# Kernel tuning notes

Hardware: AMD Instinct MI355X
Metric: run time of the kernel (lower is better)

Reference implementation:

```python
import jax, jax.numpy as jnp
import numpy as np
from functools import partial

B, DIN, H, D, HW = 4096, 2048, 1024, 256, 256
MAX_STEPS = 15
STEP = 1.0 / MAX_STEPS
WEIGHT = 1.0


def safe_norm(x):
    # per-sample L2 norm, keepdims, nan-safe at 0
    return jnp.sqrt(jnp.sum(x * x, axis=-1, keepdims=True) + 1e-24)


def setup_inputs() -> dict:
    key = jax.random.key(0)
    ks = jax.random.split(key, 16)
    s = lambda fan: 1.0 / np.sqrt(fan)
    inp = {
        'x_start': jax.random.normal(ks[0], (B, DIN), jnp.float32),
        'x_end': jax.random.normal(ks[1], (B, DIN), jnp.float32),
        'noise_raw': jax.random.normal(ks[2], (B, D), jnp.float32),
        # encoder params
        'W1': jax.random.normal(ks[3], (DIN, H), jnp.float32) * s(DIN),
        'b1': jnp.zeros((H,), jnp.float32),
        'W2': jax.random.normal(ks[4], (H, D), jnp.float32) * s(H),
        'b2': jnp.zeros((D,), jnp.float32),
        # Zermelo wind field params
        'Ww1': jax.random.normal(ks[5], (D, HW), jnp.float32) * s(D),
        'bw1': jnp.zeros((HW,), jnp.float32),
        'Ww2': jax.random.normal(ks[6], (HW, D), jnp.float32) * s(HW),
        'bw2': jnp.zeros((D,), jnp.float32),
        # conformal potential phi params (metric g = exp(phi) I)
        'Wp1': jax.random.normal(ks[7], (D, HW), jnp.float32) * s(D),
        'bp1': jnp.zeros((HW,), jnp.float32),
        'wp2': jax.random.normal(ks[8], (HW,), jnp.float32) * s(HW),
    }
    return inp


def _encode(x, W1, b1, W2, b2):
    return jnp.tanh(x @ W1 + b1) @ W2 + b2  # [B, D]


def _wind(z, Ww1, bw1, Ww2, bw2):
    return jnp.tanh(z @ Ww1 + bw1) @ Ww2 + bw2  # [B, D]


def _grad_phi(x, Wp1, bp1, wp2):
    # phi(x) = wp2 . tanh(x @ Wp1 + bp1); analytic gradient, fully vectorized
    h = jnp.tanh(x @ Wp1 + bp1)          # [B, HW]
    return ((1.0 - h * h) * wp2) @ Wp1.T  # [B, D]


def _accel(x, v, Wp1, bp1, wp2):
    # geodesic spray of conformal metric e^{phi} I:
    # a = -(grad_phi . v) v + 0.5 |v|^2 grad_phi
    g = _grad_phi(x, Wp1, bp1, wp2)
    gv = jnp.sum(g * v, axis=-1, keepdims=True)
    vv = jnp.sum(v * v, axis=-1, keepdims=True)
    return -gv * v + 0.5 * vv * g


def _trace(z0, v0, Wp1, bp1, wp2):
    h = STEP
    acc = partial(_accel, Wp1=Wp1, bp1=bp1, wp2=wp2)

    def step(carry, _):
        x, v = carry
        k1x, k1v = v, acc(x, v)
        k2x, k2v = v + 0.5 * h * k1v, acc(x + 0.5 * h * k1x, v + 0.5 * h * k1v)
        k3x, k3v = v + 0.5 * h * k2v, acc(x + 0.5 * h * k2x, v + 0.5 * h * k2v)
        k4x, k4v = v + h * k3v, acc(x + h * k3x, v + h * k3v)
        xn = x + (h / 6.0) * (k1x + 2 * k2x + 2 * k3x + k4x)
        vn = v + (h / 6.0) * (k1v + 2 * k2v + 2 * k3v + k4v)
        return (xn, vn), xn

    (_, _), xs = jax.lax.scan(step, (z0, v0), None, length=MAX_STEPS)
    return xs  # [MAX_STEPS, B, D] == xs[1:] of the original trace


def reference(x_start, x_end, noise_raw, W1, b1, W2, b2,
              Ww1, bw1, Ww2, bw2, Wp1, bp1, wp2):
    z_s = _encode(x_start, W1, b1, W2, b2)
    z_e = _encode(x_end, W1, b1, W2, b2)
    W_start = _wind(z_s, Ww1, bw1, Ww2, bw2)
    # degenerate-wind fallback: tiny tangent noise (Euclidean manifold -> identity projection)
    noise = noise_raw / (safe_norm(noise_raw) + 1e-12) * 1e-4
    w_norm = safe_norm(W_start)  # [B, 1]
    W_start = jnp.where(w_norm < 1e-5, W_start + noise, W_start)
    xs = _trace(z_s, W_start, Wp1, bp1, wp2)          # [S, B, D]
    dists_sq = jnp.sum((xs - z_e) ** 2, axis=-1)      # [S, B]
    min_dist_sq = jnp.min(dists_sq, axis=0)           # closest approach per sample
    return jnp.mean(min_dist_sq) * WEIGHT
```

## Files before the change

kernel.cpp:

```cpp
#include <hip/hip_runtime.h>
#include <math.h>

typedef short bf8 __attribute__((ext_vector_type(8)));
typedef short s4v __attribute__((ext_vector_type(4)));
typedef float f32x4 __attribute__((ext_vector_type(4)));

namespace {

constexpr float H_STEP = 1.0f / 15.0f;

__device__ inline short f2bf(float f) {
  unsigned u = __float_as_uint(f);
  u += 0x7fffu + ((u >> 16) & 1u);
  return (short)(u >> 16);
}

__device__ inline float fast_tanh(float x) {
  const float ax = fabsf(x);
  const float e = __expf(-2.0f * ax);
  const float t = (1.0f - e) * __builtin_amdgcn_rcpf(1.0f + e);
  return copysignf(t, x);
}

__device__ inline float sech2(float x) {
  const float e = __expf(-2.0f * fabsf(x));
  const float r = __builtin_amdgcn_rcpf(1.0f + e);
  return 4.0f * e * r * r;
}

template <int CTRL>
__device__ inline float dppadd(float v) {
  return v + __int_as_float(__builtin_amdgcn_update_dpp(
                 0, __float_as_int(v), CTRL, 0xF, 0xF, true));
}
__device__ inline float red16(float v) {
  v = dppadd<0x121>(v);
  v = dppadd<0x122>(v);
  v = dppadd<0x124>(v);
  v = dppadd<0x128>(v);
  return v;
}

__device__ inline void async16(const void* g, void* l) {
  __builtin_amdgcn_global_load_lds((__attribute__((address_space(1))) void*)g,
                                   (__attribute__((address_space(3))) void*)l,
                                   16, 0, 0);
}

__device__ inline void stpk4(short* base, int byteoff, float a, float b,
                             float c, float d) {
  unsigned lo, hi;
  asm("v_cvt_pk_bf16_f32 %0, %1, %2" : "=v"(lo) : "v"(a), "v"(b));
  asm("v_cvt_pk_bf16_f32 %0, %1, %2" : "=v"(hi) : "v"(c), "v"(d));
  uint2 u;
  u.x = lo;
  u.y = hi;
  *(uint2*)((char*)base + byteoff) = u;
}

__global__ __launch_bounds__(256) void prep_all(
    const float* __restrict__ xs, const float* __restrict__ xe,
    const float* __restrict__ W1, const float* __restrict__ W2,
    const float* __restrict__ Ww1, const float* __restrict__ Ww2,
    const float* __restrict__ Wp1, const float* __restrict__ wp2,
    short* __restrict__ XSb, short* __restrict__ W1T, short* __restrict__ W2T,
    short* __restrict__ Ww1T, short* __restrict__ Ww2T,
    short* __restrict__ WpT, short* __restrict__ Wp1s,
    float* __restrict__ outz) {
  __shared__ float tile[32][33];
  const int id = blockIdx.x;
  if (id < 2048) {
    if (id == 0 && threadIdx.x == 0) *outz = 0.0f;
    const long n = (long)8192 * 2048, half = n >> 1;
    long i = ((long)id * 256 + threadIdx.x) * 4;
    const long stride = (long)2048 * 1024;
    for (; i < n; i += stride) {
      const float* s = (i < half) ? (xs + i) : (xe + (i - half));
      const float4 f = *(const float4*)s;
      ushort4 o;
      o.x = (unsigned short)f2bf(f.x);
      o.y = (unsigned short)f2bf(f.y);
      o.z = (unsigned short)f2bf(f.z);
      o.w = (unsigned short)f2bf(f.w);
      *(ushort4*)(XSb + i) = o;
    }
    return;
  }
  const int tr = threadIdx.x >> 5, tc = threadIdx.x & 31;
  const float* src;
  short* dst;
  int K, N, kt, nt;
  if (id < 4096) {
    src = W1; dst = W1T; K = 2048; N = 1024; kt = (id - 2048) >> 5; nt = (id - 2048) & 31;
  } else if (id < 4352) {
    src = W2; dst = W2T; K = 1024; N = 256; kt = (id - 4096) >> 3; nt = (id - 4096) & 7;
  } else if (id < 4416) {
    src = Ww1; dst = Ww1T; K = 256; N = 256; kt = (id - 4352) >> 3; nt = (id - 4352) & 7;
  } else if (id < 4480) {
    src = Ww2; dst = Ww2T; K = 256; N = 256; kt = (id - 4416) >> 3; nt = (id - 4416) & 7;
  } else if (id < 4544) {
    src = Wp1; dst = WpT; K = 256; N = 256; kt = (id - 4480) >> 3; nt = (id - 4480) & 7;
  } else {
    const int lid = id - 4544;
    const int k0 = (lid >> 3) * 32, n0 = (lid & 7) * 32;
#pragma unroll
    for (int i = 0; i < 32; i += 8) {
      const size_t o = (size_t)(k0 + tr + i) * 256 + n0 + tc;
      Wp1s[o] = f2bf(Wp1[o] * wp2[n0 + tc]);
    }
    return;
  }
  const int k0 = kt * 32, n0 = nt * 32;
#pragma unroll
  for (int i = 0; i < 32; i += 8)
    tile[tr + i][tc] = src[(size_t)(k0 + tr + i) * N + n0 + tc];
  __syncthreads();
#pragma unroll
  for (int i = 0; i < 32; i += 8)
    dst[(size_t)(n0 + tr + i) * K + k0 + tc] = f2bf(tile[tc][tr + i]);
}


__global__ __launch_bounds__(256) void gemm128_tanh(
    const short* __restrict__ A, const short* __restrict__ Bt,
    const float* __restrict__ bias, short* __restrict__ Cb, int M, int N,
    int K) {
  __shared__ __align__(16) short As[2 * 128 * 32];
  __shared__ __align__(16) short Bs[2 * 128 * 32];
  const int tid = threadIdx.x;
  const int w = tid >> 6, lane = tid & 63, q = lane >> 4, l15 = lane & 15;
  const int wm = (w >> 1) * 64, wn = (w & 1) * 64;
  const int m0 = blockIdx.y * 128, n0 = blockIdx.x * 128;
  const f32x4 fzero = {0.0f, 0.0f, 0.0f, 0.0f};
  f32x4 acc[4][4];
#pragma unroll
  for (int mt = 0; mt < 4; ++mt)
#pragma unroll
    for (int nt = 0; nt < 4; ++nt) acc[mt][nt] = fzero;

  for (int k0 = 0; k0 < K; k0 += 64) {
#pragma unroll
    for (int kcb = 0; kcb < 2; ++kcb)
#pragma unroll
      for (int j = 0; j < 2; ++j) {
        const int c = w * 128 + j * 64 + lane;
        async16(A + (size_t)(m0 + (c >> 2)) * K + k0 + kcb * 32 + (c & 3) * 8,
                &As[kcb * 4096 + (w * 128 + j * 64) * 8]);
        async16(Bt + (size_t)(n0 + (c >> 2)) * K + k0 + kcb * 32 + (c & 3) * 8,
                &Bs[kcb * 4096 + (w * 128 + j * 64) * 8]);
      }
    __syncthreads();
#pragma unroll
    for (int kcb = 0; kcb < 2; ++kcb) {
      bf8 af[4], bfr[4];
#pragma unroll
      for (int mt = 0; mt < 4; ++mt)
        af[mt] =
            *(const bf8*)&As[kcb * 4096 + (wm + mt * 16 + l15) * 32 + q * 8];
#pragma unroll
      for (int nt = 0; nt < 4; ++nt)
        bfr[nt] =
            *(const bf8*)&Bs[kcb * 4096 + (wn + nt * 16 + l15) * 32 + q * 8];
#pragma unroll
      for (int mt = 0; mt < 4; ++mt)
#pragma unroll
        for (int nt = 0; nt < 4; ++nt)
          acc[mt][nt] = __builtin_amdgcn_mfma_f32_16x16x32_bf16(
              af[mt], bfr[nt], acc[mt][nt], 0, 0, 0);
    }
    __syncthreads();
  }
#pragma unroll
  for (int mt = 0; mt < 4; ++mt)
#pragma unroll
    for (int nt = 0; nt < 4; ++nt) {
      const int col = n0 + wn + nt * 16 + l15;
      const float bcol = bias[col];
#pragma unroll
      for (int rg = 0; rg < 4; ++rg) {
        const int row = m0 + wm + mt * 16 + q * 4 + rg;
        Cb[(size_t)row * N + col] = f2bf(fast_tanh(acc[mt][nt][rg] + bcol));
      }
    }
}

__global__ __launch_bounds__(256) void gemm64_enc2(
    const short* __restrict__ A, const short* __restrict__ Bt,
    const float* __restrict__ bias, float* __restrict__ Zs,
    float* __restrict__ Ze, int M, int N, int K) {
  __shared__ __align__(16) short As[2 * 64 * 32];
  __shared__ __align__(16) short Bs[2 * 64 * 32];
  const int tid = threadIdx.x;
  const int w = tid >> 6, lane = tid & 63, q = lane >> 4, l15 = lane & 15;
  const int wm = (w >> 1) * 32, wn = (w & 1) * 32;
  const int m0 = blockIdx.y * 64, n0 = blockIdx.x * 64;
  const f32x4 fzero = {0.0f, 0.0f, 0.0f, 0.0f};
  f32x4 acc[2][2];
#pragma unroll
  for (int mt = 0; mt < 2; ++mt)
#pragma unroll
    for (int nt = 0; nt < 2; ++nt) acc[mt][nt] = fzero;

  for (int k0 = 0; k0 < K; k0 += 64) {
    const int c = w * 64 + lane;
#pragma unroll
    for (int kcb = 0; kcb < 2; ++kcb) {
      async16(A + (size_t)(m0 + (c >> 2)) * K + k0 + kcb * 32 + (c & 3) * 8,
              &As[kcb * 2048 + (w * 64) * 8]);
      async16(Bt + (size_t)(n0 + (c >> 2)) * K + k0 + kcb * 32 + (c & 3) * 8,
              &Bs[kcb * 2048 + (w * 64) * 8]);
    }
    __syncthreads();
#pragma unroll
    for (int kcb = 0; kcb < 2; ++kcb) {
      bf8 af[2], bfr[2];
#pragma unroll
      for (int mt = 0; mt < 2; ++mt)
        af[mt] =
            *(const bf8*)&As[kcb * 2048 + (wm + mt * 16 + l15) * 32 + q * 8];
#pragma unroll
      for (int nt = 0; nt < 2; ++nt)
        bfr[nt] =
            *(const bf8*)&Bs[kcb * 2048 + (wn + nt * 16 + l15) * 32 + q * 8];
#pragma unroll
      for (int mt = 0; mt < 2; ++mt)
#pragma unroll
        for (int nt = 0; nt < 2; ++nt)
          acc[mt][nt] = __builtin_amdgcn_mfma_f32_16x16x32_bf16(
              af[mt], bfr[nt], acc[mt][nt], 0, 0, 0);
    }
    __syncthreads();
  }
#pragma unroll
  for (int mt = 0; mt < 2; ++mt)
#pragma unroll
    for (int nt = 0; nt < 2; ++nt) {
      const int col = n0 + wn + nt * 16 + l15;
      const float bcol = bias[col];
#pragma unroll
      for (int rg = 0; rg < 4; ++rg) {
        const int row = m0 + wm + mt * 16 + q * 4 + rg;
        const float val = acc[mt][nt][rg] + bcol;
        if (row < 4096)
          Zs[(size_t)row * N + col] = val;
        else
          Ze[(size_t)(row - 4096) * N + col] = val;
      }
    }
}


__global__ __launch_bounds__(512, 2) void trace_fused(
    const float* __restrict__ Xg, const float* __restrict__ ZEg,
    const float* __restrict__ NZg, const short* __restrict__ WT,
    const short* __restrict__ Wp1s, const short* __restrict__ Ww1T,
    const short* __restrict__ Ww2T, const float* __restrict__ bw1,
    const float* __restrict__ bw2, const float* __restrict__ bp1,
    float* __restrict__ out) {
  constexpr float hs = H_STEP;
  __shared__ __align__(16) short XsL[4096];
  __shared__ __align__(16) short UL[4096];
  __shared__ __align__(16) float gvv[2][16][2];
  __shared__ __align__(16) float db[2][16];
  const int tid = threadIdx.x;
  const int w = tid >> 6, lane = tid & 63, q = lane >> 4, l15 = lane & 15;
  const int r0 = blockIdx.x * 16;
  const int col0 = w * 32 + q * 4;
  const int wrow = w * 32 + l15;

  if (tid < 16) {
    *(float2*)gvv[0][tid] = make_float2(0.f, 0.f);
    *(float2*)gvv[1][tid] = make_float2(0.f, 0.f);
    db[0][tid] = 0.f;
    db[1][tid] = 0.f;
  }

  const int smask = ((l15 >> 1) & 7) ^ ((l15 & 1) << 2);
  int wadrT[2], radrT[8];
#pragma unroll
  for (int t = 0; t < 2; ++t) {
    const int slot = w * 4 + t * 2 + (q >> 1);
    wadrT[t] = (l15 * 32 + (slot ^ smask)) * 16 + (q & 1) * 8;
  }
#pragma unroll
  for (int ks = 0; ks < 8; ++ks)
    radrT[ks] = (l15 * 32 + ((ks * 4 + q) ^ smask)) * 16;

  float x[2][4], ze[2][4], nz[2][4];
#pragma unroll
  for (int t = 0; t < 2; ++t) {
    const size_t off = (size_t)(r0 + l15) * 256 + col0 + t * 16;
    const float4 xa = *(const float4*)(Xg + off);
    const float4 za = *(const float4*)(ZEg + off);
    const float4 na = *(const float4*)(NZg + off);
    x[t][0] = xa.x; x[t][1] = xa.y; x[t][2] = xa.z; x[t][3] = xa.w;
    ze[t][0] = za.x; ze[t][1] = za.y; ze[t][2] = za.z; ze[t][3] = za.w;
    nz[t][0] = na.x; nz[t][1] = na.y; nz[t][2] = na.z; nz[t][3] = na.w;
  }
  float bp1c[2][4];
#pragma unroll
  for (int t = 0; t < 2; ++t) {
    const float4 pa = *(const float4*)(bp1 + col0 + t * 16);
    bp1c[t][0] = pa.x; bp1c[t][1] = pa.y; bp1c[t][2] = pa.z; bp1c[t][3] = pa.w;
  }
  const f32x4 fzero = {0.0f, 0.0f, 0.0f, 0.0f};

  float v[2][4];
  {
    bf8 Wf1[2][8], Wf2[2][8];
#pragma unroll
    for (int t = 0; t < 2; ++t)
#pragma unroll
      for (int ks = 0; ks < 8; ++ks) {
        Wf1[t][ks] =
            *(const bf8*)(Ww1T + (size_t)(wrow + t * 16) * 256 + ks * 32 + q * 8);
        Wf2[t][ks] =
            *(const bf8*)(Ww2T + (size_t)(wrow + t * 16) * 256 + ks * 32 + q * 8);
      }
    float bw1c[2][4], bw2c[2][4];
#pragma unroll
    for (int t = 0; t < 2; ++t) {
      const float4 a1 = *(const float4*)(bw1 + col0 + t * 16);
      const float4 a2 = *(const float4*)(bw2 + col0 + t * 16);
      bw1c[t][0] = a1.x; bw1c[t][1] = a1.y; bw1c[t][2] = a1.z; bw1c[t][3] = a1.w;
      bw2c[t][0] = a2.x; bw2c[t][1] = a2.y; bw2c[t][2] = a2.z; bw2c[t][3] = a2.w;
    }
#pragma unroll
    for (int t = 0; t < 2; ++t)
      stpk4(XsL, wadrT[t], x[t][0], x[t][1], x[t][2], x[t][3]);
    __syncthreads();
    bf8 af[8];
#pragma unroll
    for (int ks = 0; ks < 8; ++ks)
      af[ks] = *(const bf8*)((const char*)XsL + radrT[ks]);
    f32x4 acc[2];
#pragma unroll
    for (int t = 0; t < 2; ++t) {
      f32x4 a0 = fzero, a1 = fzero;
#pragma unroll
      for (int ks = 0; ks < 8; ks += 2) {
        a0 = __builtin_amdgcn_mfma_f32_16x16x32_bf16(Wf1[t][ks], af[ks], a0, 0,
                                                     0, 0);
        a1 = __builtin_amdgcn_mfma_f32_16x16x32_bf16(Wf1[t][ks + 1],
                                                     af[ks + 1], a1, 0, 0, 0);
      }
      acc[t] = a0 + a1;
    }
#pragma unroll
    for (int t = 0; t < 2; ++t)
      stpk4(UL, wadrT[t], fast_tanh(acc[t][0] + bw1c[t][0]),
            fast_tanh(acc[t][1] + bw1c[t][1]),
            fast_tanh(acc[t][2] + bw1c[t][2]),
            fast_tanh(acc[t][3] + bw1c[t][3]));
    __syncthreads();
#pragma unroll
    for (int ks = 0; ks < 8; ++ks)
      af[ks] = *(const bf8*)((const char*)UL + radrT[ks]);
#pragma unroll
    for (int t = 0; t < 2; ++t) {
      f32x4 a0 = fzero, a1 = fzero;
#pragma unroll
      for (int ks = 0; ks < 8; ks += 2) {
        a0 = __builtin_amdgcn_mfma_f32_16x16x32_bf16(Wf2[t][ks], af[ks], a0, 0,
                                                     0, 0);
        a1 = __builtin_amdgcn_mfma_f32_16x16x32_bf16(Wf2[t][ks + 1],
                                                     af[ks + 1], a1, 0, 0, 0);
      }
      acc[t] = a0 + a1;
#pragma unroll
      for (int rg = 0; rg < 4; ++rg) v[t][rg] = acc[t][rg] + bw2c[t][rg];
    }
    float pn = 0.f, pm = 0.f;
#pragma unroll
    for (int t = 0; t < 2; ++t)
#pragma unroll
      for (int rg = 0; rg < 4; ++rg) {
        pn = fmaf(v[t][rg], v[t][rg], pn);
        pm = fmaf(nz[t][rg], nz[t][rg], pm);
      }
    pn += __shfl_xor(pn, 16);
    pn += __shfl_xor(pn, 32);
    pm += __shfl_xor(pm, 16);
    pm += __shfl_xor(pm, 32);
    if (q == 0) {
      atomicAdd(&gvv[0][l15][0], pn);
      atomicAdd(&gvv[0][l15][1], pm);
    }
    __syncthreads();
    const float wn = sqrtf(gvv[0][l15][0] + 1e-24f);
    const float sc =
        (wn < 1e-5f) ? 1e-4f / (sqrtf(gvv[0][l15][1] + 1e-24f) + 1e-12f) : 0.0f;
#pragma unroll
    for (int t = 0; t < 2; ++t)
#pragma unroll
      for (int rg = 0; rg < 4; ++rg) v[t][rg] = fmaf(sc, nz[t][rg], v[t][rg]);
    __syncthreads();
    if (tid < 16) *(float2*)gvv[0][tid] = make_float2(0.f, 0.f);
    __syncthreads();
  }

  bf8 B1f[2][8], B2f[2][8];
#pragma unroll
  for (int t = 0; t < 2; ++t)
#pragma unroll
    for (int ks = 0; ks < 8; ++ks) {
      B1f[t][ks] =
          *(const bf8*)(WT + (size_t)(wrow + t * 16) * 256 + ks * 32 + q * 8);
      B2f[t][ks] =
          *(const bf8*)(Wp1s + (size_t)(wrow + t * 16) * 256 + ks * 32 + q * 8);
    }
  float ap[2][4], xacc[2][4], vacc[2][4];
#pragma unroll
  for (int t = 0; t < 2; ++t)
#pragma unroll
    for (int rg = 0; rg < 4; ++rg) ap[t][rg] = 0.0f;
  float md = 3.4e38f;
  const float cxv_t[4] = {0.0f, 0.5f * hs, 0.5f * hs, hs};
  const float cxa_t[4] = {0.0f, 0.0f, 0.25f * hs * hs, 0.5f * hs * hs};
  const float cva_t[4] = {0.0f, 0.5f * hs, 0.5f * hs, hs};

#pragma unroll 1
  for (int step = 0; step < 15; ++step) {
#pragma unroll
    for (int st = 0; st < 4; ++st) {
      const int p = st & 1;
      const float cxv = cxv_t[st], cxa = cxa_t[st], cva = cva_t[st];
      float vs[2][4], pv = 0.f;
#pragma unroll
      for (int t = 0; t < 2; ++t) {
        float sx[4];
#pragma unroll
        for (int rg = 0; rg < 4; ++rg) {
          vs[t][rg] = fmaf(cva, ap[t][rg], v[t][rg]);
          sx[rg] = x[t][rg] + cxv * v[t][rg] + cxa * ap[t][rg];
          pv = fmaf(vs[t][rg], vs[t][rg], pv);
        }
        stpk4(XsL, wadrT[t], sx[0], sx[1], sx[2], sx[3]);
      }
      pv += __shfl_xor(pv, 16);
      pv += __shfl_xor(pv, 32);
      if (q == 0) atomicAdd(&gvv[p][l15][1], pv);
      __syncthreads();
      if (st == 0 && step > 0) md = fminf(md, db[(step - 1) & 1][l15]);
      bf8 af[8];
#pragma unroll
      for (int ks = 0; ks < 8; ++ks)
        af[ks] = *(const bf8*)((const char*)XsL + radrT[ks]);
      f32x4 acc[2];
#pragma unroll
      for (int t = 0; t < 2; ++t) {
        f32x4 a0 = fzero, a1 = fzero;
#pragma unroll
        for (int ks = 0; ks < 8; ks += 2) {
          a0 = __builtin_amdgcn_mfma_f32_16x16x32_bf16(B1f[t][ks], af[ks], a0,
                                                       0, 0, 0);
          a1 = __builtin_amdgcn_mfma_f32_16x16x32_bf16(B1f[t][ks + 1],
                                                       af[ks + 1], a1, 0, 0,
                                                       0);
        }
        acc[t] = a0 + a1;
        stpk4(UL, wadrT[t], sech2(acc[t][0] + bp1c[t][0]),
              sech2(acc[t][1] + bp1c[t][1]), sech2(acc[t][2] + bp1c[t][2]),
              sech2(acc[t][3] + bp1c[t][3]));
      }
      if (tid < 16) *(float2*)gvv[p ^ 1][tid] = make_float2(0.f, 0.f);
      __syncthreads();
      if (st == 0 && step > 0 && tid < 16) db[(step - 1) & 1][tid] = 0.0f;
#pragma unroll
      for (int ks = 0; ks < 8; ++ks)
        af[ks] = *(const bf8*)((const char*)UL + radrT[ks]);
#pragma unroll
      for (int t = 0; t < 2; ++t) {
        f32x4 a0 = fzero, a1 = fzero;
#pragma unroll
        for (int ks = 0; ks < 8; ks += 2) {
          a0 = __builtin_amdgcn_mfma_f32_16x16x32_bf16(B2f[t][ks], af[ks], a0,
                                                       0, 0, 0);
          a1 = __builtin_amdgcn_mfma_f32_16x16x32_bf16(B2f[t][ks + 1],
                                                       af[ks + 1], a1, 0, 0,
                                                       0);
        }
        acc[t] = a0 + a1;
      }
      float pg = 0.f;
#pragma unroll
      for (int t = 0; t < 2; ++t)
#pragma unroll
        for (int rg = 0; rg < 4; ++rg) pg = fmaf(acc[t][rg], vs[t][rg], pg);
      pg += __shfl_xor(pg, 16);
      pg += __shfl_xor(pg, 32);
      if (q == 0) atomicAdd(&gvv[p][l15][0], pg);
      __syncthreads();
      const float2 r2 = *(const float2*)gvv[p][l15];
      const float gv = r2.x, vv = r2.y;
#pragma unroll
      for (int t = 0; t < 2; ++t)
#pragma unroll
        for (int rg = 0; rg < 4; ++rg) {
          const float a = -gv * vs[t][rg] + 0.5f * vv * acc[t][rg];
          ap[t][rg] = a;
          if (st == 0) {
            xacc[t][rg] = a;
            vacc[t][rg] = a;
          } else if (st < 3) {
            xacc[t][rg] += a;
            vacc[t][rg] += 2.0f * a;
          } else {
            vacc[t][rg] += a;
          }
        }
      if (st == 3) {
        const int sp = step & 1;
        float pd = 0.f;
#pragma unroll
        for (int t = 0; t < 2; ++t)
#pragma unroll
          for (int rg = 0; rg < 4; ++rg) {
            const float xn =
                x[t][rg] + hs * v[t][rg] + (hs * hs / 6.0f) * xacc[t][rg];
            const float vn = v[t][rg] + (hs / 6.0f) * vacc[t][rg];
            x[t][rg] = xn;
            v[t][rg] = vn;
            const float dd = xn - ze[t][rg];
            pd = fmaf(dd, dd, pd);
          }
        pd += __shfl_xor(pd, 16);
        pd += __shfl_xor(pd, 32);
        if (q == 0) atomicAdd(&db[sp][l15], pd);
      }
    }
  }
  __syncthreads();
  md = fminf(md, db[14 & 1][l15]);
  if (w == 0) {
    const float s = red16(md);
    if (tid == 0) atomicAdd(out, s * (1.0f / 4096.0f));
  }
}

}

extern "C" void kernel_launch(void* const* d_in, const int* in_sizes, int n_in,
                              void* d_out, int out_size, void* d_ws,
                              size_t ws_size, hipStream_t stream) {
  (void)in_sizes; (void)n_in; (void)out_size; (void)ws_size;
  const float* x_start = (const float*)d_in[0];
  const float* x_end = (const float*)d_in[1];
  const float* noise = (const float*)d_in[2];
  const float* W1 = (const float*)d_in[3];
  const float* b1 = (const float*)d_in[4];
  const float* W2 = (const float*)d_in[5];
  const float* b2 = (const float*)d_in[6];
  const float* Ww1 = (const float*)d_in[7];
  const float* bw1 = (const float*)d_in[8];
  const float* Ww2 = (const float*)d_in[9];
  const float* bw2 = (const float*)d_in[10];
  const float* Wp1 = (const float*)d_in[11];
  const float* bp1 = (const float*)d_in[12];
  const float* wp2 = (const float*)d_in[13];
  float* out = (float*)d_out;

  float* Xf = (float*)d_ws;
  float* ZEf = Xf + (size_t)4096 * 256;
  short* XSb = (short*)(ZEf + (size_t)4096 * 256);
  short* H1b = XSb + (size_t)8192 * 2048;
  short* W1T = H1b + (size_t)8192 * 1024;
  short* W2T = W1T + (size_t)1024 * 2048;
  short* Ww1T = W2T + (size_t)256 * 1024;
  short* Ww2T = Ww1T + 65536;
  short* WpT = Ww2T + 65536;
  short* Wp1s = WpT + 65536;

  const dim3 blk(256);

  prep_all<<<4608, blk, 0, stream>>>(x_start, x_end, W1, W2, Ww1, Ww2, Wp1,
                                     wp2, XSb, W1T, W2T, Ww1T, Ww2T, WpT,
                                     Wp1s, out);
  gemm128_tanh<<<dim3(8, 64), blk, 0, stream>>>(XSb, W1T, b1, H1b, 8192, 1024,
                                                2048);
  gemm64_enc2<<<dim3(4, 128), blk, 0, stream>>>(H1b, W2T, b2, Xf, ZEf, 8192,
                                                256, 1024);
  trace_fused<<<256, dim3(512), 0, stream>>>(Xf, ZEf, noise, WpT, Wp1s, Ww1T,
                                             Ww2T, bw1, bw2, bp1, out);
}
```

Before: 315.7 us.

## Split trace_fused work across 16 waves with one 16-column tile each

Doubles the trace kernel's block size from 512 to 1024 threads, so each wave owns one 16-column output tile instead of two. This halves per-thread register state (weight fragments, x/v accumulators) and doubles the number of waves available to hide MFMA and LDS latency within the sequential RK4 loop. In exchange, every barrier and shared-memory atomic reduction now synchronises 16 waves instead of 8, and launch bounds request 4 waves per SIMD, which limits registers per thread.

New measurement: 349.6 us. +10.7%, slower.

```diff
diff --git a/kernel.cpp b/kernel.cpp
--- a/kernel.cpp
+++ b/kernel.cpp
@@ -2,7 +2,6 @@
 #include <math.h>
 
 typedef short bf8 __attribute__((ext_vector_type(8)));
-typedef short s4v __attribute__((ext_vector_type(4)));
 typedef float f32x4 __attribute__((ext_vector_type(4)));
 
 namespace {
@@ -250,7 +249,7 @@
 }
 
 
-__global__ __launch_bounds__(512, 2) void trace_fused(
+__global__ __launch_bounds__(1024, 4) void trace_fused(
     const float* __restrict__ Xg, const float* __restrict__ ZEg,
     const float* __restrict__ NZg, const short* __restrict__ WT,
     const short* __restrict__ Wp1s, const short* __restrict__ Ww1T,
@@ -265,8 +264,8 @@
   const int tid = threadIdx.x;
   const int w = tid >> 6, lane = tid & 63, q = lane >> 4, l15 = lane & 15;
   const int r0 = blockIdx.x * 16;
-  const int col0 = w * 32 + q * 4;
-  const int wrow = w * 32 + l15;
+  const int col0 = w * 16 + q * 4;
+  const int wrow = w * 16 + l15;
 
   if (tid < 16) {
     *(float2*)gvv[0][tid] = make_float2(0.f, 0.f);
@@ -276,108 +275,88 @@
   }
 
   const int smask = ((l15 >> 1) & 7) ^ ((l15 & 1) << 2);
-  int wadrT[2], radrT[8];
-#pragma unroll
-  for (int t = 0; t < 2; ++t) {
-    const int slot = w * 4 + t * 2 + (q >> 1);
-    wadrT[t] = (l15 * 32 + (slot ^ smask)) * 16 + (q & 1) * 8;
-  }
+  const int wadr =
+      (l15 * 32 + ((w * 2 + (q >> 1)) ^ smask)) * 16 + (q & 1) * 8;
+  int radrT[8];
 #pragma unroll
   for (int ks = 0; ks < 8; ++ks)
     radrT[ks] = (l15 * 32 + ((ks * 4 + q) ^ smask)) * 16;
 
-  float x[2][4], ze[2][4], nz[2][4];
-#pragma unroll
-  for (int t = 0; t < 2; ++t) {
-    const size_t off = (size_t)(r0 + l15) * 256 + col0 + t * 16;
+  float x[4], ze[4], nz[4];
+  {
+    const size_t off = (size_t)(r0 + l15) * 256 + col0;
     const float4 xa = *(const float4*)(Xg + off);
     const float4 za = *(const float4*)(ZEg + off);
     const float4 na = *(const float4*)(NZg + off);
-    x[t][0] = xa.x; x[t][1] = xa.y; x[t][2] = xa.z; x[t][3] = xa.w;
-    ze[t][0] = za.x; ze[t][1] = za.y; ze[t][2] = za.z; ze[t][3] = za.w;
-    nz[t][0] = na.x; nz[t][1] = na.y; nz[t][2] = na.z; nz[t][3] = na.w;
-  }
-  float bp1c[2][4];
-#pragma unroll
-  for (int t = 0; t < 2; ++t) {
-    const float4 pa = *(const float4*)(bp1 + col0 + t * 16);
-    bp1c[t][0] = pa.x; bp1c[t][1] = pa.y; bp1c[t][2] = pa.z; bp1c[t][3] = pa.w;
+    x[0] = xa.x; x[1] = xa.y; x[2] = xa.z; x[3] = xa.w;
+    ze[0] = za.x; ze[1] = za.y; ze[2] = za.z; ze[3] = za.w;
+    nz[0] = na.x; nz[1] = na.y; nz[2] = na.z; nz[3] = na.w;
+  }
+  float bp1c[4];
+  {
+    const float4 pa = *(const float4*)(bp1 + col0);
+    bp1c[0] = pa.x; bp1c[1] = pa.y; bp1c[2] = pa.z; bp1c[3] = pa.w;
   }
   const f32x4 fzero = {0.0f, 0.0f, 0.0f, 0.0f};
 
-  float v[2][4];
+  float v[4];
   {
-    bf8 Wf1[2][8], Wf2[2][8];
-#pragma unroll
-    for (int t = 0; t < 2; ++t)
-#pragma unroll
-      for (int ks = 0; ks < 8; ++ks) {
-        Wf1[t][ks] =
-            *(const bf8*)(Ww1T + (size_t)(wrow + t * 16) * 256 + ks * 32 + q * 8);
-        Wf2[t][ks] =
-            *(const bf8*)(Ww2T + (size_t)(wrow + t * 16) * 256 + ks * 32 + q * 8);
-      }
-    float bw1c[2][4], bw2c[2][4];
-#pragma unroll
-    for (int t = 0; t < 2; ++t) {
-      const float4 a1 = *(const float4*)(bw1 + col0 + t * 16);
-      const float4 a2 = *(const float4*)(bw2 + col0 + t * 16);
-      bw1c[t][0] = a1.x; bw1c[t][1] = a1.y; bw1c[t][2] = a1.z; bw1c[t][3] = a1.w;
-      bw2c[t][0] = a2.x; bw2c[t][1] = a2.y; bw2c[t][2] = a2.z; bw2c[t][3] = a2.w;
-    }
-#pragma unroll
-    for (int t = 0; t < 2; ++t)
-      stpk4(XsL, wadrT[t], x[t][0], x[t][1], x[t][2], x[t][3]);
+    bf8 Wf1[8], Wf2[8];
+#pragma unroll
+    for (int ks = 0; ks < 8; ++ks) {
+      Wf1[ks] = *(const bf8*)(Ww1T + (size_t)wrow * 256 + ks * 32 + q * 8);
+      Wf2[ks] = *(const bf8*)(Ww2T + (size_t)wrow * 256 + ks * 32 + q * 8);
+    }
+    float bw1c[4], bw2c[4];
+    {
+      const float4 a1 = *(const float4*)(bw1 + col0);
+      const float4 a2 = *(const float4*)(bw2 + col0);
+      bw1c[0] = a1.x; bw1c[1] = a1.y; bw1c[2] = a1.z; bw1c[3] = a1.w;
+      bw2c[0] = a2.x; bw2c[1] = a2.y; bw2c[2] = a2.z; bw2c[3] = a2.w;
+    }
+    stpk4(XsL, wadr, x[0], x[1], x[2], x[3]);
     __syncthreads();
     bf8 af[8];
 #pragma unroll
     for (int ks = 0; ks < 8; ++ks)
       af[ks] = *(const bf8*)((const char*)XsL + radrT[ks]);
-    f32x4 acc[2];
-#pragma unroll
-    for (int t = 0; t < 2; ++t) {
+    f32x4 acc;
+    {
       f32x4 a0 = fzero, a1 = fzero;
 #pragma unroll
       for (int ks = 0; ks < 8; ks += 2) {
-        a0 = __builtin_amdgcn_mfma_f32_16x16x32_bf16(Wf1[t][ks], af[ks], a0, 0,
+        a0 = __builtin_amdgcn_mfma_f32_16x16x32_bf16(Wf1[ks], af[ks], a0, 0,
                                                      0, 0);
-        a1 = __builtin_amdgcn_mfma_f32_16x16x32_bf16(Wf1[t][ks + 1],
-                                                     af[ks + 1], a1, 0, 0, 0);
-      }
-      acc[t] = a0 + a1;
-    }
-#pragma unroll
-    for (int t = 0; t < 2; ++t)
-      stpk4(UL, wadrT[t], fast_tanh(acc[t][0] + bw1c[t][0]),
-            fast_tanh(acc[t][1] + bw1c[t][1]),
-            fast_tanh(acc[t][2] + bw1c[t][2]),
-            fast_tanh(acc[t][3] + bw1c[t][3]));
+        a1 = __builtin_amdgcn_mfma_f32_16x16x32_bf16(Wf1[ks + 1], af[ks + 1],
+                                                     a1, 0, 0, 0);
+      }
+      acc = a0 + a1;
+    }
+    stpk4(UL, wadr, fast_tanh(acc[0] + bw1c[0]), fast_tanh(acc[1] + bw1c[1]),
+          fast_tanh(acc[2] + bw1c[2]), fast_tanh(acc[3] + bw1c[3]));
     __syncthreads();
 #pragma unroll
     for (int ks = 0; ks < 8; ++ks)
       af[ks] = *(const bf8*)((const char*)UL + radrT[ks]);
-#pragma unroll
-    for (int t = 0; t < 2; ++t) {
+    {
       f32x4 a0 = fzero, a1 = fzero;
 #pragma unroll
       for (int ks = 0; ks < 8; ks += 2) {
-        a0 = __builtin_amdgcn_mfma_f32_16x16x32_bf16(Wf2[t][ks], af[ks], a0, 0,
+        a0 = __builtin_amdgcn_mfma_f32_16x16x32_bf16(Wf2[ks], af[ks], a0, 0,
                                                      0, 0);
-        a1 = __builtin_amdgcn_mfma_f32_16x16x32_bf16(Wf2[t][ks + 1],
-                                                     af[ks + 1], a1, 0, 0, 0);
-      }
-      acc[t] = a0 + a1;
-#pragma unroll
-      for (int rg = 0; rg < 4; ++rg) v[t][rg] = acc[t][rg] + bw2c[t][rg];
-    }
+        a1 = __builtin_amdgcn_mfma_f32_16x16x32_bf16(Wf2[ks + 1], af[ks + 1],
+                                                     a1, 0, 0, 0);
+      }
+      acc = a0 + a1;
+    }
+#pragma unroll
+    for (int rg = 0; rg < 4; ++rg) v[rg] = acc[rg] + bw2c[rg];
     float pn = 0.f, pm = 0.f;
 #pragma unroll
-    for (int t = 0; t < 2; ++t)
-#pragma unroll
-      for (int rg = 0; rg < 4; ++rg) {
-        pn = fmaf(v[t][rg], v[t][rg], pn);
-        pm = fmaf(nz[t][rg], nz[t][rg], pm);
-      }
+    for (int rg = 0; rg < 4; ++rg) {
+      pn = fmaf(v[rg], v[rg], pn);
+      pm = fmaf(nz[rg], nz[rg], pm);
+    }
     pn += __shfl_xor(pn, 16);
     pn += __shfl_xor(pn, 32);
     pm += __shfl_xor(pm, 16);
@@ -391,29 +370,21 @@
     const float sc =
         (wn < 1e-5f) ? 1e-4f / (sqrtf(gvv[0][l15][1] + 1e-24f) + 1e-12f) : 0.0f;
 #pragma unroll
-    for (int t = 0; t < 2; ++t)
-#pragma unroll
-      for (int rg = 0; rg < 4; ++rg) v[t][rg] = fmaf(sc, nz[t][rg], v[t][rg]);
+    for (int rg = 0; rg < 4; ++rg) v[rg] = fmaf(sc, nz[rg], v[rg]);
     __syncthreads();
     if (tid < 16) *(float2*)gvv[0][tid] = make_float2(0.f, 0.f);
     __syncthreads();
   }
 
-  bf8 B1f[2][8], B2f[2][8];
-#pragma unroll
-  for (int t = 0; t < 2; ++t)
-#pragma unroll
-    for (int ks = 0; ks < 8; ++ks) {
-      B1f[t][ks] =
-          *(const bf8*)(WT + (size_t)(wrow + t * 16) * 256 + ks * 32 + q * 8);
-      B2f[t][ks] =
-          *(const bf8*)(Wp1s + (size_t)(wrow + t * 16) * 256 + ks * 32 + q * 8);
-    }
-  float ap[2][4], xacc[2][4], vacc[2][4];
-#pragma unroll
-  for (int t = 0; t < 2; ++t)
-#pragma unroll
-    for (int rg = 0; rg < 4; ++rg) ap[t][rg] = 0.0f;
+  bf8 B1f[8], B2f[8];
+#pragma unroll
+  for (int ks = 0; ks < 8; ++ks) {
+    B1f[ks] = *(const bf8*)(WT + (size_t)wrow * 256 + ks * 32 + q * 8);
+    B2f[ks] = *(const bf8*)(Wp1s + (size_t)wrow * 256 + ks * 32 + q * 8);
+  }
+  float ap[4], xacc[4], vacc[4];
+#pragma unroll
+  for (int rg = 0; rg < 4; ++rg) ap[rg] = 0.0f;
   float md = 3.4e38f;
   const float cxv_t[4] = {0.0f, 0.5f * hs, 0.5f * hs, hs};
   const float cxa_t[4] = {0.0f, 0.0f, 0.25f * hs * hs, 0.5f * hs * hs};
@@ -425,17 +396,16 @@
     for (int st = 0; st < 4; ++st) {
       const int p = st & 1;
       const float cxv = cxv_t[st], cxa = cxa_t[st], cva = cva_t[st];
-      float vs[2][4], pv = 0.f;
-#pragma unroll
-      for (int t = 0; t < 2; ++t) {
+      float vs[4], pv = 0.f;
+      {
         float sx[4];
 #pragma unroll
         for (int rg = 0; rg < 4; ++rg) {
-          vs[t][rg] = fmaf(cva, ap[t][rg], v[t][rg]);
-          sx[rg] = x[t][rg] + cxv * v[t][rg] + cxa * ap[t][rg];
-          pv = fmaf(vs[t][rg], vs[t][rg], pv);
+          vs[rg] = fmaf(cva, ap[rg], v[rg]);
+          sx[rg] = x[rg] + cxv * v[rg] + cxa * ap[rg];
+          pv = fmaf(vs[rg], vs[rg], pv);
         }
-        stpk4(XsL, wadrT[t], sx[0], sx[1], sx[2], sx[3]);
+        stpk4(XsL, wadr, sx[0], sx[1], sx[2], sx[3]);
       }
       pv += __shfl_xor(pv, 16);
       pv += __shfl_xor(pv, 32);
@@ -446,47 +416,42 @@
 #pragma unroll
       for (int ks = 0; ks < 8; ++ks)
         af[ks] = *(const bf8*)((const char*)XsL + radrT[ks]);
-      f32x4 acc[2];
-#pragma unroll
-      for (int t = 0; t < 2; ++t) {
+      f32x4 acc;
+      {
         f32x4 a0 = fzero, a1 = fzero;
 #pragma unroll
         for (int ks = 0; ks < 8; ks += 2) {
-          a0 = __builtin_amdgcn_mfma_f32_16x16x32_bf16(B1f[t][ks], af[ks], a0,
-                                                       0, 0, 0);
-          a1 = __builtin_amdgcn_mfma_f32_16x16x32_bf16(B1f[t][ks + 1],
+          a0 = __builtin_amdgcn_mfma_f32_16x16x32_bf16(B1f[ks], af[ks], a0, 0,
+                                                       0, 0);
+          a1 = __builtin_amdgcn_mfma_f32_16x16x32_bf16(B1f[ks + 1],
                                                        af[ks + 1], a1, 0, 0,
                                                        0);
         }
-        acc[t] = a0 + a1;
-        stpk4(UL, wadrT[t], sech2(acc[t][0] + bp1c[t][0]),
-              sech2(acc[t][1] + bp1c[t][1]), sech2(acc[t][2] + bp1c[t][2]),
-              sech2(acc[t][3] + bp1c[t][3]));
-      }
+        acc = a0 + a1;
+      }
+      stpk4(UL, wadr, sech2(acc[0] + bp1c[0]), sech2(acc[1] + bp1c[1]),
+            sech2(acc[2] + bp1c[2]), sech2(acc[3] + bp1c[3]));
       if (tid < 16) *(float2*)gvv[p ^ 1][tid] = make_float2(0.f, 0.f);
       __syncthreads();
       if (st == 0 && step > 0 && tid < 16) db[(step - 1) & 1][tid] = 0.0f;
 #pragma unroll
       for (int ks = 0; ks < 8; ++ks)
         af[ks] = *(const bf8*)((const char*)UL + radrT[ks]);
-#pragma unroll
-      for (int t = 0; t < 2; ++t) {
+      {
         f32x4 a0 = fzero, a1 = fzero;
 #pragma unroll
         for (int ks = 0; ks < 8; ks += 2) {
-          a0 = __builtin_amdgcn_mfma_f32_16x16x32_bf16(B2f[t][ks], af[ks], a0,
-                                                       0, 0, 0);
-          a1 = __builtin_amdgcn_mfma_f32_16x16x32_bf16(B2f[t][ks + 1],
+          a0 = __builtin_amdgcn_mfma_f32_16x16x32_bf16(B2f[ks], af[ks], a0, 0,
+                                                       0, 0);
+          a1 = __builtin_amdgcn_mfma_f32_16x16x32_bf16(B2f[ks + 1],
                                                        af[ks + 1], a1, 0, 0,
                                                        0);
         }
-        acc[t] = a0 + a1;
+        acc = a0 + a1;
       }
       float pg = 0.f;
 #pragma unroll
-      for (int t = 0; t < 2; ++t)
-#pragma unroll
-        for (int rg = 0; rg < 4; ++rg) pg = fmaf(acc[t][rg], vs[t][rg], pg);
+      for (int rg = 0; rg < 4; ++rg) pg = fmaf(acc[rg], vs[rg], pg);
       pg += __shfl_xor(pg, 16);
       pg += __shfl_xor(pg, 32);
       if (q == 0) atomicAdd(&gvv[p][l15][0], pg);
@@ -494,36 +459,31 @@
       const float2 r2 = *(const float2*)gvv[p][l15];
       const float gv = r2.x, vv = r2.y;
 #pragma unroll
-      for (int t = 0; t < 2; ++t)
-#pragma unroll
-        for (int rg = 0; rg < 4; ++rg) {
-          const float a = -gv * vs[t][rg] + 0.5f * vv * acc[t][rg];
-          ap[t][rg] = a;
-          if (st == 0) {
-            xacc[t][rg] = a;
-            vacc[t][rg] = a;
-          } else if (st < 3) {
-            xacc[t][rg] += a;
-            vacc[t][rg] += 2.0f * a;
-          } else {
-            vacc[t][rg] += a;
-          }
+      for (int rg = 0; rg < 4; ++rg) {
+        const float a = -gv * vs[rg] + 0.5f * vv * acc[rg];
+        ap[rg] = a;
+        if (st == 0) {
+          xacc[rg] = a;
+          vacc[rg] = a;
+        } else if (st < 3) {
+          xacc[rg] += a;
+          vacc[rg] += 2.0f * a;
+        } else {
+          vacc[rg] += a;
         }
+      }
       if (st == 3) {
         const int sp = step & 1;
         float pd = 0.f;
 #pragma unroll
-        for (int t = 0; t < 2; ++t)
-#pragma unroll
-          for (int rg = 0; rg < 4; ++rg) {
-            const float xn =
-                x[t][rg] + hs * v[t][rg] + (hs * hs / 6.0f) * xacc[t][rg];
-            const float vn = v[t][rg] + (hs / 6.0f) * vacc[t][rg];
-            x[t][rg] = xn;
-            v[t][rg] = vn;
-            const float dd = xn - ze[t][rg];
-            pd = fmaf(dd, dd, pd);
-          }
+        for (int rg = 0; rg < 4; ++rg) {
+          const float xn = x[rg] + hs * v[rg] + (hs * hs / 6.0f) * xacc[rg];
+          const float vn = v[rg] + (hs / 6.0f) * vacc[rg];
+          x[rg] = xn;
+          v[rg] = vn;
+          const float dd = xn - ze[rg];
+          pd = fmaf(dd, dd, pd);
+        }
         pd += __shfl_xor(pd, 16);
         pd += __shfl_xor(pd, 32);
         if (q == 0) atomicAdd(&db[sp][l15], pd);
@@ -580,6 +540,6 @@
                                                 2048);
   gemm64_enc2<<<dim3(4, 128), blk, 0, stream>>>(H1b, W2T, b2, Xf, ZEf, 8192,
                                                 256, 1024);
-  trace_fused<<<256, dim3(512), 0, stream>>>(Xf, ZEf, noise, WpT, Wp1s, Ww1T,
-                                             Ww2T, bw1, bw2, bp1, out);
-}
+  trace_fused<<<256, dim3(1024), 0, stream>>>(Xf, ZEf, noise, WpT, Wp1s, Ww1T,
+                                              Ww2T, bw1, bw2, bp1, out);
+}
```

## Stage scaled Wp1 weights in LDS instead of holding them in registers

Applied to the files above, without the earlier changes.

The second-stage weight fragments (Wp1 scaled by wp2) used in the gradient GEMM of every RK4 stage are no longer held as 16 bf8 register tiles per thread. Prep lays them out in a swizzled LDS-friendly order, each block copies them asynchronously into 128KB of dynamic shared memory, and the fragments are read from LDS inside the inner loop. This frees a large number of VGPRs to relieve register pressure or spilling, at the cost of extra LDS reads per MFMA and a much larger shared-memory footprint per block, which can limit blocks per CU.

Result: slower. 333.2 us (+5.5%).

```diff
diff --git a/kernel.cpp b/kernel.cpp
--- a/kernel.cpp
+++ b/kernel.cpp
@@ -2,12 +2,12 @@
 #include <math.h>
 
 typedef short bf8 __attribute__((ext_vector_type(8)));
-typedef short s4v __attribute__((ext_vector_type(4)));
 typedef float f32x4 __attribute__((ext_vector_type(4)));
 
 namespace {
 
 constexpr float H_STEP = 1.0f / 15.0f;
+constexpr int SMEM_BYTES = 131072 + 8192 + 8192 + 256 + 128;
 
 __device__ inline short f2bf(float f) {
   unsigned u = __float_as_uint(f);
@@ -65,7 +65,7 @@
     const float* __restrict__ Wp1, const float* __restrict__ wp2,
     short* __restrict__ XSb, short* __restrict__ W1T, short* __restrict__ W2T,
     short* __restrict__ Ww1T, short* __restrict__ Ww2T,
-    short* __restrict__ WpT, short* __restrict__ Wp1s,
+    short* __restrict__ WpT, short* __restrict__ Wp1L,
     float* __restrict__ outz) {
   __shared__ float tile[32][33];
   const int id = blockIdx.x;
@@ -102,12 +102,22 @@
     src = Wp1; dst = WpT; K = 256; N = 256; kt = (id - 4480) >> 3; nt = (id - 4480) & 7;
   } else {
     const int lid = id - 4544;
-    const int k0 = (lid >> 3) * 32, n0 = (lid & 7) * 32;
-#pragma unroll
-    for (int i = 0; i < 32; i += 8) {
-      const size_t o = (size_t)(k0 + tr + i) * 256 + n0 + tc;
-      Wp1s[o] = f2bf(Wp1[o] * wp2[n0 + tc]);
-    }
+    const int L = (lid * 256 + threadIdx.x) * 4;
+    const int slice = L >> 12;
+    const int within = L & 4095;
+    const int r15 = within >> 8;
+    const int slotp = (within >> 3) & 31;
+    const int h = within & 7;
+    const int sm = ((r15 >> 1) & 7) ^ ((r15 & 1) << 2);
+    const int col = ((slotp ^ sm) << 3) + h;
+    const int row = slice * 16 + r15;
+    const float* wrow_p = Wp1 + (size_t)row * 256 + col;
+    ushort4 o;
+    o.x = (unsigned short)f2bf(wrow_p[0] * wp2[col + 0]);
+    o.y = (unsigned short)f2bf(wrow_p[1] * wp2[col + 1]);
+    o.z = (unsigned short)f2bf(wrow_p[2] * wp2[col + 2]);
+    o.w = (unsigned short)f2bf(wrow_p[3] * wp2[col + 3]);
+    *(ushort4*)(Wp1L + L) = o;
     return;
   }
   const int k0 = kt * 32, n0 = nt * 32;
@@ -253,20 +263,27 @@
 __global__ __launch_bounds__(512, 2) void trace_fused(
     const float* __restrict__ Xg, const float* __restrict__ ZEg,
     const float* __restrict__ NZg, const short* __restrict__ WT,
-    const short* __restrict__ Wp1s, const short* __restrict__ Ww1T,
+    const short* __restrict__ Wp1Lg, const short* __restrict__ Ww1T,
     const short* __restrict__ Ww2T, const float* __restrict__ bw1,
     const float* __restrict__ bw2, const float* __restrict__ bp1,
     float* __restrict__ out) {
   constexpr float hs = H_STEP;
-  __shared__ __align__(16) short XsL[4096];
-  __shared__ __align__(16) short UL[4096];
-  __shared__ __align__(16) float gvv[2][16][2];
-  __shared__ __align__(16) float db[2][16];
+  extern __shared__ __align__(16) char smem[];
+  short* W2L = (short*)smem;
+  short* XsL = (short*)(smem + 131072);
+  short* UL = (short*)(smem + 139264);
+  float(*gvv)[16][2] = (float(*)[16][2])(smem + 147456);
+  float(*db)[16] = (float(*)[16])(smem + 147712);
   const int tid = threadIdx.x;
   const int w = tid >> 6, lane = tid & 63, q = lane >> 4, l15 = lane & 15;
   const int r0 = blockIdx.x * 16;
   const int col0 = w * 32 + q * 4;
   const int wrow = w * 32 + l15;
+
+#pragma unroll
+  for (int it = 0; it < 16; ++it)
+    async16((const char*)Wp1Lg + (it * 8 + w) * 1024 + lane * 16,
+            (char*)W2L + (it * 8 + w) * 1024);
 
   if (tid < 16) {
     *(float2*)gvv[0][tid] = make_float2(0.f, 0.f);
@@ -399,15 +416,14 @@
     __syncthreads();
   }
 
-  bf8 B1f[2][8], B2f[2][8];
+  bf8 B1f[2][8];
 #pragma unroll
   for (int t = 0; t < 2; ++t)
 #pragma unroll
     for (int ks = 0; ks < 8; ++ks) {
       B1f[t][ks] =
           *(const bf8*)(WT + (size_t)(wrow + t * 16) * 256 + ks * 32 + q * 8);
-      B2f[t][ks] =
-          *(const bf8*)(Wp1s + (size_t)(wrow + t * 16) * 256 + ks * 32 + q * 8);
+      asm volatile("" : "+v"(B1f[t][ks]));
     }
   float ap[2][4], xacc[2][4], vacc[2][4];
 #pragma unroll
@@ -471,14 +487,16 @@
         af[ks] = *(const bf8*)((const char*)UL + radrT[ks]);
 #pragma unroll
       for (int t = 0; t < 2; ++t) {
+        const char* wb = (const char*)W2L + (w * 2 + t) * 8192;
         f32x4 a0 = fzero, a1 = fzero;
 #pragma unroll
         for (int ks = 0; ks < 8; ks += 2) {
-          a0 = __builtin_amdgcn_mfma_f32_16x16x32_bf16(B2f[t][ks], af[ks], a0,
-                                                       0, 0, 0);
-          a1 = __builtin_amdgcn_mfma_f32_16x16x32_bf16(B2f[t][ks + 1],
-                                                       af[ks + 1], a1, 0, 0,
+          const bf8 b0 = *(const bf8*)(wb + radrT[ks]);
+          const bf8 b1 = *(const bf8*)(wb + radrT[ks + 1]);
+          a0 = __builtin_amdgcn_mfma_f32_16x16x32_bf16(b0, af[ks], a0, 0, 0,
                                                        0);
+          a1 = __builtin_amdgcn_mfma_f32_16x16x32_bf16(b1, af[ks + 1], a1, 0,
+                                                       0, 0);
         }
         acc[t] = a0 + a1;
       }
@@ -569,17 +587,25 @@
   short* Ww1T = W2T + (size_t)256 * 1024;
   short* Ww2T = Ww1T + 65536;
   short* WpT = Ww2T + 65536;
-  short* Wp1s = WpT + 65536;
+  short* Wp1L = WpT + 65536;
+
+  static bool cfg = false;
+  if (!cfg) {
+    hipFuncSetAttribute(reinterpret_cast<const void*>(&trace_fused),
+                        hipFuncAttributeMaxDynamicSharedMemorySize,
+                        SMEM_BYTES);
+    cfg = true;
+  }
 
   const dim3 blk(256);
 
   prep_all<<<4608, blk, 0, stream>>>(x_start, x_end, W1, W2, Ww1, Ww2, Wp1,
                                      wp2, XSb, W1T, W2T, Ww1T, Ww2T, WpT,
-                                     Wp1s, out);
+                                     Wp1L, out);
   gemm128_tanh<<<dim3(8, 64), blk, 0, stream>>>(XSb, W1T, b1, H1b, 8192, 1024,
                                                 2048);
   gemm64_enc2<<<dim3(4, 128), blk, 0, stream>>>(H1b, W2T, b2, Xf, ZEf, 8192,
                                                 256, 1024);
-  trace_fused<<<256, dim3(512), 0, stream>>>(Xf, ZEf, noise, WpT, Wp1s, Ww1T,
-                                             Ww2T, bw1, bw2, bp1, out);
-}
+  trace_fused<<<256, dim3(512), SMEM_BYTES, stream>>>(
+      Xf, ZEf, noise, WpT, Wp1L, Ww1T, Ww2T, bw1, bw2, bp1, out);
+}
```
